# Optimization experiments

Hardware: AMD Instinct MI355X
Metric: run time of the kernel (lower is better)

Reference implementation:

```python
import jax, jax.numpy as jnp
import numpy as np

N = 50000   # nodes
E = 800000  # edges
IN, HID, OUT, H = 128, 256, 128, 4
C1 = HID // H  # per-head channels for conv1/conv2
EPS_LN = 1e-5


def layer_norm(x, g, b):
    mu = x.mean(-1, keepdims=True)
    var = ((x - mu) ** 2).mean(-1, keepdims=True)
    return (x - mu) * jax.lax.rsqrt(var + EPS_LN) * g + b


def gatv2(x, src, dst, edge_attr, Wl, bl, Wr, br, We, att, bias, heads, ch, n):
    # PyG GATv2Conv (concat=True, negative_slope=0.2, share_weights=False)
    xl = (x @ Wl + bl).reshape(-1, heads, ch)   # [N,H,C] source transform
    xr = (x @ Wr + br).reshape(-1, heads, ch)   # [N,H,C] target transform
    e = (edge_attr @ We).reshape(-1, heads, ch) # [E,H,C] edge transform (no bias)
    m = jax.nn.leaky_relu(xl[src] + xr[dst] + e, 0.2)     # [E,H,C]
    logits = jnp.einsum('ehc,hc->eh', m, att)             # [E,H]
    mx = jax.ops.segment_max(logits, dst, num_segments=n) # segment softmax over dst
    a = jnp.exp(logits - mx[dst])
    denom = jax.ops.segment_sum(a, dst, num_segments=n)
    alpha = a / (denom[dst] + 1e-16)                      # [E,H]
    out = jax.ops.segment_sum(xl[src] * alpha[..., None], dst, num_segments=n)
    return out.reshape(-1, heads * ch) + bias


def setup_inputs() -> dict:
    key = jax.random.key(0)
    ks = jax.random.split(key, 24)
    s = 0.05
    inp = {
        'x': jax.random.normal(ks[0], (N, IN), jnp.float32),
        'edge_index': jax.random.randint(ks[1], (2, E), 0, N, jnp.int32),
        'edge_attr': jax.random.uniform(ks[2], (E, 1), jnp.float32),
        # conv1: in=IN, out per head=C1, heads=H
        'Wl1': jax.random.normal(ks[3], (IN, HID)) * s,  'bl1': jnp.zeros((HID,)),
        'Wr1': jax.random.normal(ks[4], (IN, HID)) * s,  'br1': jnp.zeros((HID,)),
        'We1': jax.random.normal(ks[5], (1, HID)) * s,
        'att1': jax.random.normal(ks[6], (H, C1)) * s,   'bo1': jnp.zeros((HID,)),
        'g1': jnp.ones((HID,)), 'be1': jnp.zeros((HID,)),
        # conv2: in=HID
        'Wl2': jax.random.normal(ks[7], (HID, HID)) * s, 'bl2': jnp.zeros((HID,)),
        'Wr2': jax.random.normal(ks[8], (HID, HID)) * s, 'br2': jnp.zeros((HID,)),
        'We2': jax.random.normal(ks[9], (1, HID)) * s,
        'att2': jax.random.normal(ks[10], (H, C1)) * s,  'bo2': jnp.zeros((HID,)),
        'g2': jnp.ones((HID,)), 'be2': jnp.zeros((HID,)),
        # conv3: heads=1, out=OUT
        'Wl3': jax.random.normal(ks[11], (HID, OUT)) * s, 'bl3': jnp.zeros((OUT,)),
        'Wr3': jax.random.normal(ks[12], (HID, OUT)) * s, 'br3': jnp.zeros((OUT,)),
        'We3': jax.random.normal(ks[13], (1, OUT)) * s,
        'att3': jax.random.normal(ks[14], (1, OUT)) * s,  'bo3': jnp.zeros((OUT,)),
        'g3': jnp.ones((OUT,)), 'be3': jnp.zeros((OUT,)),
    }
    return inp


def reference(x, edge_index, edge_attr,
              Wl1, bl1, Wr1, br1, We1, att1, bo1, g1, be1,
              Wl2, bl2, Wr2, br2, We2, att2, bo2, g2, be2,
              Wl3, bl3, Wr3, br3, We3, att3, bo3, g3, be3):
    src, dst = edge_index[0], edge_index[1]
    h = gatv2(x, src, dst, edge_attr, Wl1, bl1, Wr1, br1, We1, att1, bo1, H, C1, N)
    h = jax.nn.elu(layer_norm(h, g1, be1))  # dropout inactive at inference
    h = gatv2(h, src, dst, edge_attr, Wl2, bl2, Wr2, br2, We2, att2, bo2, H, C1, N)
    h = jax.nn.elu(layer_norm(h, g2, be2))
    h = gatv2(h, src, dst, edge_attr, Wl3, bl3, Wr3, br3, We3, att3, bo3, 1, OUT, N)
    return layer_norm(h, g3, be3)
```

## Files before the change

### kernel.cpp

```cpp
#include <hip/hip_runtime.h>
#include <cstdint>
#include <cstddef>

typedef unsigned short u16;
typedef __attribute__((ext_vector_type(8))) short short8v;
typedef __attribute__((ext_vector_type(4))) float f32x4;

#define IN_DIM 128
#define HID_DIM 256
#define OUT_DIM 128
#define HEADS 4

__device__ __forceinline__ float b2f(u16 v) {
    return __uint_as_float(((unsigned)v) << 16);
}
__device__ __forceinline__ u16 f2b(float f) {
    unsigned u = __float_as_uint(f);
    u += 0x7fffu + ((u >> 16) & 1u);
    return (u16)(u >> 16);
}


__global__ void count_k(const int* __restrict__ dst, int* __restrict__ counts, int ne) {
    int i = blockIdx.x * blockDim.x + threadIdx.x;
    if (i < ne) atomicAdd(&counts[dst[i]], 1);
}

__global__ __launch_bounds__(1024) void scan_k(const int* __restrict__ counts,
                                               int* __restrict__ offs,
                                               int* __restrict__ cursor, int n) {
    __shared__ int wtot[16];
    __shared__ int carry_s;
    int tid = threadIdx.x, wv = tid >> 6, ln = tid & 63;
    if (tid == 0) carry_s = 0;
    __syncthreads();
    for (int base = 0; base < n; base += 4096) {
        int i0 = base + tid * 4;
        int4 c4 = {0, 0, 0, 0};
        if (i0 + 3 < n) c4 = *(const int4*)(counts + i0);
        else {
            if (i0     < n) c4.x = counts[i0];
            if (i0 + 1 < n) c4.y = counts[i0 + 1];
            if (i0 + 2 < n) c4.z = counts[i0 + 2];
            if (i0 + 3 < n) c4.w = counts[i0 + 3];
        }
        int s0 = c4.x, s1 = s0 + c4.y, s2 = s1 + c4.z, s3 = s2 + c4.w;
        int v = s3;
#pragma unroll
        for (int o = 1; o < 64; o <<= 1) {
            int t = __shfl_up(v, o);
            if (ln >= o) v += t;
        }
        if (ln == 63) wtot[wv] = v;
        int wpref = v - s3;
        __syncthreads();
        if (wv == 0) {
            int w2 = (ln < 16) ? wtot[ln] : 0;
#pragma unroll
            for (int o = 1; o < 16; o <<= 1) {
                int t = __shfl_up(w2, o);
                if (ln >= o) w2 += t;
            }
            if (ln < 16) wtot[ln] = w2;
        }
        __syncthreads();
        int wbase = carry_s + (wv ? wtot[wv - 1] : 0);
        int ex0 = wbase + wpref;
        if (i0     < n) { offs[i0]     = ex0;      cursor[i0]     = ex0; }
        if (i0 + 1 < n) { offs[i0 + 1] = ex0 + s0; cursor[i0 + 1] = ex0 + s0; }
        if (i0 + 2 < n) { offs[i0 + 2] = ex0 + s1; cursor[i0 + 2] = ex0 + s1; }
        if (i0 + 3 < n) { offs[i0 + 3] = ex0 + s2; cursor[i0 + 3] = ex0 + s2; }
        __syncthreads();
        if (tid == 0) carry_s += wtot[15];
        __syncthreads();
    }
    if (threadIdx.x == 0) offs[n] = carry_s;
}

__global__ void fill_k(const int* __restrict__ src, const int* __restrict__ dst,
                       const float* __restrict__ ea, int* __restrict__ cursor,
                       int* __restrict__ csrc, float* __restrict__ cea, int ne) {
    int i = blockIdx.x * blockDim.x + threadIdx.x;
    if (i < ne) {
        int p = atomicAdd(&cursor[dst[i]], 1);
        csrc[p] = src[i];
        cea[p] = ea[i];
    }
}


template <int KG>
__global__ void xpack_k(const float* __restrict__ X, short* __restrict__ Xp, int total) {
    int gid = blockIdx.x * blockDim.x + threadIdx.x;
    if (gid >= total) return;
    int lane = gid & 63;
    int kg = (gid >> 6) % KG;
    int rt = gid / (64 * KG);
    int row = rt * 16 + (lane & 15);
    int k0 = kg * 32 + ((lane >> 4) << 3);
    const float* src = X + (size_t)row * (KG * 32) + k0;
    short8v o;
#pragma unroll
    for (int j = 0; j < 8; j++) o[j] = (short)f2b(src[j]);
    ((short8v*)Xp)[gid] = o;
}

template <int K, int HOUT>
__global__ void packw_k(const float* __restrict__ Wl, const float* __restrict__ Wr,
                        short* __restrict__ Wp) {
    constexpr int KG = K / 32;
    int gid = blockIdx.x * blockDim.x + threadIdx.x;
    int lane = gid & 63;
    int kg = (gid >> 6) % KG;
    int nt = gid / (64 * KG);
    int col = nt * 16 + (lane & 15);
    int k0 = kg * 32 + ((lane >> 4) << 3);
    const float* Wsrc = (col < HOUT) ? Wl : Wr;
    int c2 = (col < HOUT) ? col : col - HOUT;
    short8v o;
#pragma unroll
    for (int j = 0; j < 8; j++) o[j] = (short)f2b(Wsrc[(size_t)(k0 + j) * HOUT + c2]);
    ((short8v*)Wp)[gid] = o;
}


template <int KG, int NT, int HOUT, int R>
__global__ __launch_bounds__(256) void gemm_mfma(
    const short* __restrict__ Xp, const short* __restrict__ Wp,
    const float* __restrict__ bl, const float* __restrict__ br,
    u16* __restrict__ XL, u16* __restrict__ XR, int nrt) {
    constexpr int NCG = NT / 8;
    int w = threadIdx.x >> 6, lane = threadIdx.x & 63;
    int cg = blockIdx.x % NCG;
    int rt0 = (blockIdx.x / NCG) * R;
    if (rt0 >= nrt) return;
    int rcnt = min(R, nrt - rt0);
    int nt0 = cg * 8 + w * 2;
    const short8v* wb = (const short8v*)Wp + lane;
    short8v wf0[KG], wf1[KG];
#pragma unroll
    for (int kg = 0; kg < KG; kg++) {
        wf0[kg] = wb[(size_t)(nt0 * KG + kg) * 64];
        wf1[kg] = wb[(size_t)((nt0 + 1) * KG + kg) * 64];
    }
    int colg0 = nt0 * 16 + ((lane >> 4) << 2);
    int colg1 = colg0 + 16;
    bool isr0 = colg0 >= HOUT;
    bool isr1 = colg1 >= HOUT;
    int cl0 = colg0 - (isr0 ? HOUT : 0);
    int cl1 = colg1 - (isr1 ? HOUT : 0);
    float4 bb0 = *(const float4*)((isr0 ? br : bl) + cl0);
    float4 bb1 = *(const float4*)((isr1 ? br : bl) + cl1);
    u16* ob0 = (isr0 ? XR : XL) + cl0;
    u16* ob1 = (isr1 ? XR : XL) + cl1;

    const short8v* xb = (const short8v*)Xp + (size_t)rt0 * KG * 64 + lane;
    for (int r = 0; r < rcnt; ++r) {
        f32x4 acc0 = {0.f, 0.f, 0.f, 0.f}, acc1 = {0.f, 0.f, 0.f, 0.f};
#pragma unroll
        for (int kg = 0; kg < KG; kg++) {
            short8v xf = xb[(size_t)(r * KG + kg) * 64];
            acc0 = __builtin_amdgcn_mfma_f32_16x16x32_bf16(wf0[kg], xf, acc0, 0, 0, 0);
            acc1 = __builtin_amdgcn_mfma_f32_16x16x32_bf16(wf1[kg], xf, acc1, 0, 0, 0);
        }
        size_t rowoff = (size_t)((rt0 + r) * 16 + (lane & 15)) * HOUT;
        ushort4 o0 = { f2b(acc0[0] + bb0.x), f2b(acc0[1] + bb0.y),
                       f2b(acc0[2] + bb0.z), f2b(acc0[3] + bb0.w) };
        *(ushort4*)(ob0 + rowoff) = o0;
        ushort4 o1 = { f2b(acc1[0] + bb1.x), f2b(acc1[1] + bb1.y),
                       f2b(acc1[2] + bb1.z), f2b(acc1[3] + bb1.w) };
        *(ushort4*)(ob1 + rowoff) = o1;
    }
}


__global__ __launch_bounds__(256) void gat_fused4(
    const int* __restrict__ offs, const int* __restrict__ csrc, const float* __restrict__ cea,
    const float* __restrict__ We, const float* __restrict__ att,
    const u16* __restrict__ XL, const u16* __restrict__ XR,
    const float* __restrict__ bo, const float* __restrict__ g, const float* __restrict__ be,
    u16* __restrict__ hp, int n) {
    __shared__ int   sS[4][64];
    __shared__ float sEA[4][64];
    int tid = threadIdx.x;
    int w = tid >> 6;
    int lane = tid & 63;
    int node = blockIdx.x * 4 + w;
    int es = lane >> 5;
    int ls = lane & 31;
    int cabs = ls * 8;
    float xr[8], wev[8], atv[8];
    {
        short8v x8 = *(const short8v*)(XR + (size_t)node * 256 + cabs);
        float4 wA = *(const float4*)(We + cabs), wB = *(const float4*)(We + cabs + 4);
        float4 aA = *(const float4*)(att + cabs), aB = *(const float4*)(att + cabs + 4);
#pragma unroll
        for (int i = 0; i < 8; i++) xr[i] = b2f((u16)x8[i]);
        wev[0] = wA.x; wev[1] = wA.y; wev[2] = wA.z; wev[3] = wA.w;
        wev[4] = wB.x; wev[5] = wB.y; wev[6] = wB.z; wev[7] = wB.w;
        atv[0] = aA.x; atv[1] = aA.y; atv[2] = aA.z; atv[3] = aA.w;
        atv[4] = aB.x; atv[5] = aB.y; atv[6] = aB.z; atv[7] = aB.w;
    }
    int b0 = offs[node], eEnd = offs[node + 1];
    float dsum = 0.f;
    float acc[8];
#pragma unroll
    for (int i = 0; i < 8; i++) acc[i] = 0.f;
    for (int base = b0; base < eEnd; base += 64) {
        int cnt = min(64, eEnd - base);
        if (lane < cnt) { sS[w][lane] = csrc[base + lane]; sEA[w][lane] = cea[base + lane]; }
        short8v r0, r1, r2;
        float e0, e1f, e2;
        bool v0, v1, v2;
        {
            int j0 = es, j1 = es + 2, j2 = es + 4;
            v0 = j0 < cnt; v1 = j1 < cnt; v2 = j2 < cnt;
            int i0 = v0 ? j0 : 0, i1 = v1 ? j1 : 0, i2 = v2 ? j2 : 0;
            e0 = sEA[w][i0]; r0 = *(const short8v*)(XL + (size_t)sS[w][i0] * 256 + cabs);
            e1f = sEA[w][i1]; r1 = *(const short8v*)(XL + (size_t)sS[w][i1] * 256 + cabs);
            e2 = sEA[w][i2]; r2 = *(const short8v*)(XL + (size_t)sS[w][i2] * 256 + cabs);
        }
        for (int r = 0; r < cnt; r += 2) {
            short8v rc = r0; float ec = e0; bool vc = v0;
            r0 = r1; e0 = e1f; v0 = v1;
            r1 = r2; e1f = e2; v1 = v2;
            int jn = r + 6 + es;
            v2 = jn < cnt;
            int idx = v2 ? jn : 0;
            e2 = sEA[w][idx];
            r2 = *(const short8v*)(XL + (size_t)sS[w][idx] * 256 + cabs);
            float x[8];
#pragma unroll
            for (int i = 0; i < 8; i++) x[i] = b2f((u16)rc[i]);
            float p = 0.f;
#pragma unroll
            for (int i = 0; i < 8; i++) {
                float t = fmaf(ec, wev[i], x[i]) + xr[i];
                t = fmaxf(t, 0.2f * t);
                p += t * atv[i];
            }
            p += __shfl_xor(p, 1);
            p += __shfl_xor(p, 2);
            p += __shfl_xor(p, 4);
            float wv2 = vc ? __expf(p) : 0.f;
            dsum += wv2;
#pragma unroll
            for (int i = 0; i < 8; i++) acc[i] += wv2 * x[i];
        }
    }
    dsum += __shfl_xor(dsum, 32);
#pragma unroll
    for (int i = 0; i < 8; i++) acc[i] += __shfl_xor(acc[i], 32);
    float inv = 1.f / (dsum + 1e-16f);
    float4 bA = *(const float4*)(bo + cabs), bB = *(const float4*)(bo + cabs + 4);
    float v[8];
    v[0] = acc[0] * inv + bA.x; v[1] = acc[1] * inv + bA.y;
    v[2] = acc[2] * inv + bA.z; v[3] = acc[3] * inv + bA.w;
    v[4] = acc[4] * inv + bB.x; v[5] = acc[5] * inv + bB.y;
    v[6] = acc[6] * inv + bB.z; v[7] = acc[7] * inv + bB.w;
    float s1 = 0.f, s2 = 0.f;
#pragma unroll
    for (int i = 0; i < 8; i++) { s1 += v[i]; s2 += v[i] * v[i]; }
#pragma unroll
    for (int o = 16; o >= 1; o >>= 1) {
        s1 += __shfl_xor(s1, o);
        s2 += __shfl_xor(s2, o);
    }
    float mu = s1 / 256.f;
    float sinv = rsqrtf(s2 / 256.f - mu * mu + 1e-5f);
    if (es == 0) {
        float4 gA = *(const float4*)(g + cabs), gB = *(const float4*)(g + cabs + 4);
        float4 eA = *(const float4*)(be + cabs), eB = *(const float4*)(be + cabs + 4);
        float gg[8] = {gA.x, gA.y, gA.z, gA.w, gB.x, gB.y, gB.z, gB.w};
        float ee[8] = {eA.x, eA.y, eA.z, eA.w, eB.x, eB.y, eB.z, eB.w};
        short8v yv;
#pragma unroll
        for (int i = 0; i < 8; i++) {
            float y = (v[i] - mu) * sinv * gg[i] + ee[i];
            y = (y > 0.f) ? y : expm1f(y);
            yv[i] = (short)f2b(y);
        }
        int kg = cabs >> 5;
        int l = (node & 15) | (((cabs >> 3) & 3) << 4);
        size_t eoff = (((size_t)(node >> 4) * 8 + kg) * 64 + l) * 8;
        *(short8v*)(hp + eoff) = yv;
    }
}


__global__ __launch_bounds__(256) void gat_fused1(
    const int* __restrict__ offs, const int* __restrict__ csrc, const float* __restrict__ cea,
    const float* __restrict__ We, const float* __restrict__ att,
    const u16* __restrict__ XL, const u16* __restrict__ XR,
    const float* __restrict__ bo, const float* __restrict__ g, const float* __restrict__ be,
    float* __restrict__ out, int n) {
    __shared__ int   sS[64];
    __shared__ float sEA[64];
    __shared__ float wd[4];
    __shared__ float wacc[4][128];
    __shared__ float wsum[2], wsq[2];
    __shared__ float smu, sinv;
    int node = blockIdx.x;
    int tid = threadIdx.x;
    int w = tid >> 6, lane = tid & 63;
    int q = lane >> 4, ls = lane & 15;
    int cb = ls * 8;
    float xr[8], wev[8], atv[8];
    {
        short8v x8 = *(const short8v*)(XR + (size_t)node * 128 + cb);
        float4 wA = *(const float4*)(We + cb), wB = *(const float4*)(We + cb + 4);
        float4 aA = *(const float4*)(att + cb), aB = *(const float4*)(att + cb + 4);
#pragma unroll
        for (int i = 0; i < 8; i++) xr[i] = b2f((u16)x8[i]);
        wev[0] = wA.x; wev[1] = wA.y; wev[2] = wA.z; wev[3] = wA.w;
        wev[4] = wB.x; wev[5] = wB.y; wev[6] = wB.z; wev[7] = wB.w;
        atv[0] = aA.x; atv[1] = aA.y; atv[2] = aA.z; atv[3] = aA.w;
        atv[4] = aB.x; atv[5] = aB.y; atv[6] = aB.z; atv[7] = aB.w;
    }
    int b0 = offs[node], e1 = offs[node + 1];
    float dsum = 0.f;
    float acc[8];
#pragma unroll
    for (int i = 0; i < 8; i++) acc[i] = 0.f;
    for (int base = b0; base < e1; base += 64) {
        int cnt = min(64, e1 - base);
        __syncthreads();
        if (tid < cnt) { sS[tid] = csrc[base + tid]; sEA[tid] = cea[base + tid]; }
        __syncthreads();
#pragma unroll 2
        for (int j0 = w * 4; j0 < cnt; j0 += 16) {
            int j = j0 + q;
            bool valid = j < cnt;
            int jj = valid ? j : j0;
            int s = sS[jj];
            float eav = sEA[jj];
            short8v xl8 = *(const short8v*)(XL + (size_t)s * 128 + cb);
            float x[8];
#pragma unroll
            for (int i = 0; i < 8; i++) x[i] = b2f((u16)xl8[i]);
            float p = 0.f;
#pragma unroll
            for (int i = 0; i < 8; i++) {
                float t = x[i] + xr[i] + eav * wev[i];
                t = fmaxf(t, 0.2f * t);
                p += t * atv[i];
            }
            p += __shfl_xor(p, 1);
            p += __shfl_xor(p, 2);
            p += __shfl_xor(p, 4);
            p += __shfl_xor(p, 8);
            float wv = valid ? __expf(p) : 0.f;
            dsum += wv;
#pragma unroll
            for (int i = 0; i < 8; i++) acc[i] += wv * x[i];
        }
    }
#pragma unroll
    for (int o = 16; o <= 32; o <<= 1) {
        dsum += __shfl_xor(dsum, o);
#pragma unroll
        for (int i = 0; i < 8; i++) acc[i] += __shfl_xor(acc[i], o);
    }
    if (q == 0) {
        float4 avA = {acc[0], acc[1], acc[2], acc[3]};
        float4 avB = {acc[4], acc[5], acc[6], acc[7]};
        *(float4*)(&wacc[w][cb]) = avA;
        *(float4*)(&wacc[w][cb + 4]) = avB;
    }
    if (lane == 0) wd[w] = dsum;
    __syncthreads();
    float v = 0.f;
    if (tid < 128) {
        float d = wd[0] + wd[1] + wd[2] + wd[3];
        float a = wacc[0][tid] + wacc[1][tid] + wacc[2][tid] + wacc[3][tid];
        v = a / (d + 1e-16f) + bo[tid];
        float s1 = v, s2 = v * v;
#pragma unroll
        for (int o = 32; o >= 1; o >>= 1) {
            s1 += __shfl_xor(s1, o);
            s2 += __shfl_xor(s2, o);
        }
        if (lane == 0) { wsum[w] = s1; wsq[w] = s2; }
    }
    __syncthreads();
    if (tid == 0) {
        float ts = wsum[0] + wsum[1];
        float tq = wsq[0] + wsq[1];
        float mu = ts / 128.f;
        smu = mu;
        sinv = rsqrtf(tq / 128.f - mu * mu + 1e-5f);
    }
    __syncthreads();
    if (tid < 128) {
        float y = (v - smu) * sinv * g[tid] + be[tid];
        out[(size_t)node * 128 + tid] = y;
    }
}


extern "C" void kernel_launch(void* const* d_in, const int* in_sizes, int n_in,
                              void* d_out, int out_size, void* d_ws, size_t ws_size,
                              hipStream_t stream) {
    const float* x  = (const float*)d_in[0];
    const int*   ei = (const int*)d_in[1];
    const float* ea = (const float*)d_in[2];
    const float *Wl1 = (const float*)d_in[3],  *bl1 = (const float*)d_in[4];
    const float *Wr1 = (const float*)d_in[5],  *br1 = (const float*)d_in[6];
    const float *We1 = (const float*)d_in[7],  *att1 = (const float*)d_in[8];
    const float *bo1 = (const float*)d_in[9],  *g1 = (const float*)d_in[10], *be1 = (const float*)d_in[11];
    const float *Wl2 = (const float*)d_in[12], *bl2 = (const float*)d_in[13];
    const float *Wr2 = (const float*)d_in[14], *br2 = (const float*)d_in[15];
    const float *We2 = (const float*)d_in[16], *att2 = (const float*)d_in[17];
    const float *bo2 = (const float*)d_in[18], *g2 = (const float*)d_in[19], *be2 = (const float*)d_in[20];
    const float *Wl3 = (const float*)d_in[21], *bl3 = (const float*)d_in[22];
    const float *Wr3 = (const float*)d_in[23], *br3 = (const float*)d_in[24];
    const float *We3 = (const float*)d_in[25], *att3 = (const float*)d_in[26];
    const float *bo3 = (const float*)d_in[27], *g3 = (const float*)d_in[28], *be3 = (const float*)d_in[29];

    int n = in_sizes[0] / IN_DIM;
    int e = in_sizes[1] / 2;
    const int* srcv = ei;
    const int* dstv = ei + e;
    int nrt = n / 16;

    char* w = (char*)d_ws;
    size_t off = 0;
    auto take = [&](size_t bytes) -> void* {
        void* p = w + off;
        off = (off + bytes + 255) & ~(size_t)255;
        return p;
    };
    int*   counts = (int*)take((size_t)n * 4);
    int*   cursor = (int*)take((size_t)n * 4);
    int*   offs   = (int*)take((size_t)(n + 1) * 4);
    int*   csrc   = (int*)take((size_t)e * 4);
    float* ceaw   = (float*)take((size_t)e * 4);
    u16*   XL     = (u16*)take((size_t)n * HID_DIM * 2);
    u16*   XR     = (u16*)take((size_t)n * HID_DIM * 2);
    short* xpack  = (short*)take((size_t)nrt * 4 * 64 * 8 * 2);
    short* hpack  = (short*)take((size_t)nrt * 8 * 64 * 8 * 2);
    short* wp1    = (short*)take((size_t)32 * 4 * 64 * 8 * 2);
    short* wp2    = (short*)take((size_t)32 * 8 * 64 * 8 * 2);
    short* wp3    = (short*)take((size_t)16 * 8 * 64 * 8 * 2);

    const int TPB = 256;
    int eb = (e + TPB - 1) / TPB;

    hipMemsetAsync(counts, 0, (size_t)n * 4, stream);
    count_k<<<eb, TPB, 0, stream>>>(dstv, counts, e);
    scan_k<<<1, 1024, 0, stream>>>(counts, offs, cursor, n);
    fill_k<<<eb, TPB, 0, stream>>>(srcv, dstv, ea, cursor, csrc, ceaw, e);

    packw_k<IN_DIM,  HID_DIM><<<32 * 4 * 64 / TPB, TPB, 0, stream>>>(Wl1, Wr1, wp1);
    packw_k<HID_DIM, HID_DIM><<<32 * 8 * 64 / TPB, TPB, 0, stream>>>(Wl2, Wr2, wp2);
    packw_k<HID_DIM, OUT_DIM><<<16 * 8 * 64 / TPB, TPB, 0, stream>>>(Wl3, Wr3, wp3);
    int xtot = nrt * 4 * 64;
    xpack_k<4><<<(xtot + TPB - 1) / TPB, TPB, 0, stream>>>(x, xpack, xtot);

    gemm_mfma<4, 32, HID_DIM, 8><<<4 * ((nrt + 7) / 8), TPB, 0, stream>>>(
        xpack, wp1, bl1, br1, XL, XR, nrt);
    gat_fused4<<<n / 4, 256, 0, stream>>>(
        offs, csrc, ceaw, We1, att1, XL, XR, bo1, g1, be1, (u16*)hpack, n);

    gemm_mfma<8, 32, HID_DIM, 8><<<4 * ((nrt + 7) / 8), TPB, 0, stream>>>(
        hpack, wp2, bl2, br2, XL, XR, nrt);
    gat_fused4<<<n / 4, 256, 0, stream>>>(
        offs, csrc, ceaw, We2, att2, XL, XR, bo2, g2, be2, (u16*)hpack, n);

    gemm_mfma<8, 16, OUT_DIM, 4><<<2 * ((nrt + 3) / 4), TPB, 0, stream>>>(
        hpack, wp3, bl3, br3, XL, XR, nrt);
    gat_fused1<<<n, 256, 0, stream>>>(
        offs, csrc, ceaw, We3, att3, XL, XR, bo3, g3, be3, (float*)d_out, n);
}
```

Baseline: 487.3 us.

## Map one wavefront per node in final GAT layer with software-prefetched gathers

```diff
diff --git a/kernel.cpp b/kernel.cpp
--- a/kernel.cpp
+++ b/kernel.cpp
@@ -294,16 +294,14 @@
     const u16* __restrict__ XL, const u16* __restrict__ XR,
     const float* __restrict__ bo, const float* __restrict__ g, const float* __restrict__ be,
     float* __restrict__ out, int n) {
-    __shared__ int   sS[64];
-    __shared__ float sEA[64];
-    __shared__ float wd[4];
-    __shared__ float wacc[4][128];
-    __shared__ float wsum[2], wsq[2];
-    __shared__ float smu, sinv;
-    int node = blockIdx.x;
+    __shared__ int   sS[4][64];
+    __shared__ float sEA[4][64];
     int tid = threadIdx.x;
-    int w = tid >> 6, lane = tid & 63;
-    int q = lane >> 4, ls = lane & 15;
+    int w = tid >> 6;
+    int lane = tid & 63;
+    int node = blockIdx.x * 4 + w;
+    int q = lane >> 4;
+    int ls = lane & 15;
     int cb = ls * 8;
     float xr[8], wev[8], atv[8];
     {
@@ -317,31 +315,41 @@
         atv[0] = aA.x; atv[1] = aA.y; atv[2] = aA.z; atv[3] = aA.w;
         atv[4] = aB.x; atv[5] = aB.y; atv[6] = aB.z; atv[7] = aB.w;
     }
-    int b0 = offs[node], e1 = offs[node + 1];
+    int b0 = offs[node], eEnd = offs[node + 1];
     float dsum = 0.f;
     float acc[8];
 #pragma unroll
     for (int i = 0; i < 8; i++) acc[i] = 0.f;
-    for (int base = b0; base < e1; base += 64) {
-        int cnt = min(64, e1 - base);
-        __syncthreads();
-        if (tid < cnt) { sS[tid] = csrc[base + tid]; sEA[tid] = cea[base + tid]; }
-        __syncthreads();
-#pragma unroll 2
-        for (int j0 = w * 4; j0 < cnt; j0 += 16) {
-            int j = j0 + q;
-            bool valid = j < cnt;
-            int jj = valid ? j : j0;
-            int s = sS[jj];
-            float eav = sEA[jj];
-            short8v xl8 = *(const short8v*)(XL + (size_t)s * 128 + cb);
+    for (int base = b0; base < eEnd; base += 64) {
+        int cnt = min(64, eEnd - base);
+        if (lane < cnt) { sS[w][lane] = csrc[base + lane]; sEA[w][lane] = cea[base + lane]; }
+        short8v r0, r1, r2;
+        float e0, e1f, e2;
+        bool v0, v1, v2;
+        {
+            int j0 = q, j1 = q + 4, j2 = q + 8;
+            v0 = j0 < cnt; v1 = j1 < cnt; v2 = j2 < cnt;
+            int i0 = v0 ? j0 : 0, i1 = v1 ? j1 : 0, i2 = v2 ? j2 : 0;
+            e0 = sEA[w][i0]; r0 = *(const short8v*)(XL + (size_t)sS[w][i0] * 128 + cb);
+            e1f = sEA[w][i1]; r1 = *(const short8v*)(XL + (size_t)sS[w][i1] * 128 + cb);
+            e2 = sEA[w][i2]; r2 = *(const short8v*)(XL + (size_t)sS[w][i2] * 128 + cb);
+        }
+        for (int r = 0; r < cnt; r += 4) {
+            short8v rc = r0; float ec = e0; bool vc = v0;
+            r0 = r1; e0 = e1f; v0 = v1;
+            r1 = r2; e1f = e2; v1 = v2;
+            int jn = r + 12 + q;
+            v2 = jn < cnt;
+            int idx = v2 ? jn : 0;
+            e2 = sEA[w][idx];
+            r2 = *(const short8v*)(XL + (size_t)sS[w][idx] * 128 + cb);
             float x[8];
 #pragma unroll
-            for (int i = 0; i < 8; i++) x[i] = b2f((u16)xl8[i]);
+            for (int i = 0; i < 8; i++) x[i] = b2f((u16)rc[i]);
             float p = 0.f;
 #pragma unroll
             for (int i = 0; i < 8; i++) {
-                float t = x[i] + xr[i] + eav * wev[i];
+                float t = fmaf(ec, wev[i], x[i]) + xr[i];
                 t = fmaxf(t, 0.2f * t);
                 p += t * atv[i];
             }
@@ -349,51 +357,53 @@
             p += __shfl_xor(p, 2);
             p += __shfl_xor(p, 4);
             p += __shfl_xor(p, 8);
-            float wv = valid ? __expf(p) : 0.f;
-            dsum += wv;
-#pragma unroll
-            for (int i = 0; i < 8; i++) acc[i] += wv * x[i];
-        }
-    }
-#pragma unroll
-    for (int o = 16; o <= 32; o <<= 1) {
-        dsum += __shfl_xor(dsum, o);
-#pragma unroll
-        for (int i = 0; i < 8; i++) acc[i] += __shfl_xor(acc[i], o);
-    }
+            float wv2 = vc ? __expf(p) : 0.f;
+            dsum += wv2;
+#pragma unroll
+            for (int i = 0; i < 8; i++) acc[i] += wv2 * x[i];
+        }
+    }
+    dsum += __shfl_xor(dsum, 32);
+    dsum += __shfl_xor(dsum, 16);
+#pragma unroll
+    for (int i = 0; i < 8; i++) {
+        acc[i] += __shfl_xor(acc[i], 32);
+        acc[i] += __shfl_xor(acc[i], 16);
+    }
+    float inv = 1.f / (dsum + 1e-16f);
+    float4 bA = *(const float4*)(bo + cb), bB = *(const float4*)(bo + cb + 4);
+    float v[8];
+    v[0] = acc[0] * inv + bA.x; v[1] = acc[1] * inv + bA.y;
+    v[2] = acc[2] * inv + bA.z; v[3] = acc[3] * inv + bA.w;
+    v[4] = acc[4] * inv + bB.x; v[5] = acc[5] * inv + bB.y;
+    v[6] = acc[6] * inv + bB.z; v[7] = acc[7] * inv + bB.w;
+    float s1 = 0.f, s2 = 0.f;
+#pragma unroll
+    for (int i = 0; i < 8; i++) { s1 += v[i]; s2 += v[i] * v[i]; }
+#pragma unroll
+    for (int o = 8; o >= 1; o >>= 1) {
+        s1 += __shfl_xor(s1, o);
+        s2 += __shfl_xor(s2, o);
+    }
+    float mu = s1 / 128.f;
+    float sinv = rsqrtf(s2 / 128.f - mu * mu + 1e-5f);
     if (q == 0) {
-        float4 avA = {acc[0], acc[1], acc[2], acc[3]};
-        float4 avB = {acc[4], acc[5], acc[6], acc[7]};
-        *(float4*)(&wacc[w][cb]) = avA;
-        *(float4*)(&wacc[w][cb + 4]) = avB;
-    }
-    if (lane == 0) wd[w] = dsum;
-    __syncthreads();
-    float v = 0.f;
-    if (tid < 128) {
-        float d = wd[0] + wd[1] + wd[2] + wd[3];
-        float a = wacc[0][tid] + wacc[1][tid] + wacc[2][tid] + wacc[3][tid];
-        v = a / (d + 1e-16f) + bo[tid];
-        float s1 = v, s2 = v * v;
-#pragma unroll
-        for (int o = 32; o >= 1; o >>= 1) {
-            s1 += __shfl_xor(s1, o);
-            s2 += __shfl_xor(s2, o);
-        }
-        if (lane == 0) { wsum[w] = s1; wsq[w] = s2; }
-    }
-    __syncthreads();
-    if (tid == 0) {
-        float ts = wsum[0] + wsum[1];
-        float tq = wsq[0] + wsq[1];
-        float mu = ts / 128.f;
-        smu = mu;
-        sinv = rsqrtf(tq / 128.f - mu * mu + 1e-5f);
-    }
-    __syncthreads();
-    if (tid < 128) {
-        float y = (v - smu) * sinv * g[tid] + be[tid];
-        out[(size_t)node * 128 + tid] = y;
+        float4 gA = *(const float4*)(g + cb), gB = *(const float4*)(g + cb + 4);
+        float4 eA = *(const float4*)(be + cb), eB = *(const float4*)(be + cb + 4);
+        float gg[8] = {gA.x, gA.y, gA.z, gA.w, gB.x, gB.y, gB.z, gB.w};
+        float ee[8] = {eA.x, eA.y, eA.z, eA.w, eB.x, eB.y, eB.z, eB.w};
+        float4 oA, oB;
+        oA.x = (v[0] - mu) * sinv * gg[0] + ee[0];
+        oA.y = (v[1] - mu) * sinv * gg[1] + ee[1];
+        oA.z = (v[2] - mu) * sinv * gg[2] + ee[2];
+        oA.w = (v[3] - mu) * sinv * gg[3] + ee[3];
+        oB.x = (v[4] - mu) * sinv * gg[4] + ee[4];
+        oB.y = (v[5] - mu) * sinv * gg[5] + ee[5];
+        oB.z = (v[6] - mu) * sinv * gg[6] + ee[6];
+        oB.w = (v[7] - mu) * sinv * gg[7] + ee[7];
+        float* op = out + (size_t)node * 128 + cb;
+        *(float4*)op = oA;
+        *(float4*)(op + 4) = oB;
     }
 }
 
@@ -469,6 +479,6 @@
 
     gemm_mfma<8, 16, OUT_DIM, 4><<<2 * ((nrt + 3) / 4), TPB, 0, stream>>>(
         hpack, wp3, bl3, br3, XL, XR, nrt);
-    gat_fused1<<<n, 256, 0, stream>>>(
+    gat_fused1<<<n / 4, 256, 0, stream>>>(
         offs, csrc, ceaw, We3, att3, XL, XR, bo3, g3, be3, (float*)d_out, n);
 }
```

After: 441.9 us. 9.3% less time.
